# Kernel optimization log

Measured on AMD Instinct MI355X. Metric: run time of the kernel, lower is better.

Reference implementation:

```python
import jax, jax.numpy as jnp
import numpy as np

nC, STEP, ROW = 28, 2, 256
COL = ROW + (nC - 1) * STEP  # 310

# 1/alpha normalization for A_pinv: count of overlapping shifted channels per column
_counts = np.zeros((COL,), np.float32)
for _i in range(nC):
    _counts[_i * STEP:_i * STEP + ROW] += 1.0
ALPHA = jnp.asarray(1.0 / _counts)  # [COL]


def conv1x1(x, w, b):
    # x: [B,C,H,W], w: [O,C], b: [O]
    return jnp.einsum('bchw,oc->bohw', x, w) + b[None, :, None, None]


def dwconv5(x, w, b):
    # depthwise 5x5, SAME padding; w: [C,1,5,5]
    out = jax.lax.conv_general_dilated(
        x, w, window_strides=(1, 1), padding='SAME',
        dimension_numbers=('NCHW', 'OIHW', 'NCHW'),
        feature_group_count=x.shape[1])
    return out + b[None, :, None, None]


def mask_guided(m, w1, b1, w2, b2, dw, db):
    m1 = conv1x1(m, w1, b1)
    attn = jax.nn.sigmoid(dwconv5(conv1x1(m1, w2, b2), dw, db))
    emb = m1 * attn + m1
    return jnp.where(emb == 0, jnp.asarray(1e-6, emb.dtype), emb)


def A_op(x, M):
    # shift-and-add: [B,28,256,256] -> [B,1,256,310]
    z = x * M
    y = jnp.zeros((x.shape[0], 1, ROW, COL), x.dtype)
    for i in range(nC):
        y = y.at[:, :, :, i * STEP:i * STEP + ROW].add(z[:, i:i + 1])
    return y


def A_pinv_op(y, M):
    # normalize then extract shifted windows: [B,1,256,310] -> [B,28,256,256]
    z = y * ALPHA  # broadcast over last dim
    x = jnp.stack([z[:, 0, :, i * STEP:i * STEP + ROW] for i in range(nC)], axis=1)
    return x * M


def setup_inputs() -> dict:
    key = jax.random.key(0)
    ks = jax.random.split(key, 16)
    B = 16
    inp = {
        'y': jax.random.normal(ks[0], (B, 1, ROW, COL), jnp.float32),
        'Phi': jax.random.uniform(ks[1], (B, nC, ROW, ROW), jnp.float32),
        'x_pre': jax.random.normal(ks[2], (B, nC, ROW, ROW), jnp.float32),
        'delta': jnp.asarray([0.1], jnp.float32),
        'mm_w1': jax.random.normal(ks[3], (nC, nC), jnp.float32) * 0.1,
        'mm_b1': jax.random.normal(ks[4], (nC,), jnp.float32) * 0.1,
        'mm_w2': jax.random.normal(ks[5], (nC, nC), jnp.float32) * 0.1,
        'mm_b2': jax.random.normal(ks[6], (nC,), jnp.float32) * 0.1,
        'mm_dw': jax.random.normal(ks[7], (nC, 1, 5, 5), jnp.float32) * 0.1,
        'mm_db': jax.random.normal(ks[8], (nC,), jnp.float32) * 0.1,
        'pv_w1': jax.random.normal(ks[9], (nC, nC), jnp.float32) * 0.1,
        'pv_b1': jax.random.normal(ks[10], (nC,), jnp.float32) * 0.1,
        'pv_w2': jax.random.normal(ks[11], (nC, nC), jnp.float32) * 0.1,
        'pv_b2': jax.random.normal(ks[12], (nC,), jnp.float32) * 0.1,
        'pv_dw': jax.random.normal(ks[13], (nC, 1, 5, 5), jnp.float32) * 0.1,
        'pv_db': jax.random.normal(ks[14], (nC,), jnp.float32) * 0.1,
    }
    return inp


def reference(y, Phi, x_pre, delta,
              mm_w1, mm_b1, mm_w2, mm_b2, mm_dw, mm_db,
              pv_w1, pv_b1, pv_w2, pv_b2, pv_dw, pv_db):
    Phi_learned = mask_guided(Phi, mm_w1, mm_b1, mm_w2, mm_b2, mm_dw, mm_db)
    temp = y - A_op(x_pre, Phi_learned)
    Phi_pinv_learned = mask_guided(Phi, pv_w1, pv_b1, pv_w2, pv_b2, pv_dw, pv_db)
    x_init = x_pre + delta * A_pinv_op(temp, Phi_pinv_learned)
    return x_init
```

## Files before the change

### kernel.cpp

```cpp
#include <hip/hip_runtime.h>
#include <hip/hip_bf16.h>
#include <cstdint>

#define NC 28
#define HW 65536
#define ROWW 256
#define COLW 310
#define BATCH 16

typedef __hip_bfloat16 bf16;

__device__ __forceinline__ float bflo(unsigned int u) { return __uint_as_float(u << 16); }
__device__ __forceinline__ float bfhi(unsigned int u) { return __uint_as_float(u & 0xffff0000u); }
__device__ __forceinline__ unsigned int pk2(float lo, float hi) {
    unsigned short l = __builtin_bit_cast(unsigned short, __float2bfloat16(lo));
    unsigned short h = __builtin_bit_cast(unsigned short, __float2bfloat16(hi));
    return (unsigned int)l | ((unsigned int)h << 16);
}
__device__ __forceinline__ unsigned int pkh(float lo, float hi) {
    auto h = __builtin_amdgcn_cvt_pkrtz(lo, hi);
    return __builtin_bit_cast(unsigned int, h);
}
__device__ __forceinline__ float h2f_lo(unsigned int u) {
    return (float)__builtin_bit_cast(_Float16, (unsigned short)(u & 0xffffu));
}
__device__ __forceinline__ float h2f_hi(unsigned int u) {
    return (float)__builtin_bit_cast(_Float16, (unsigned short)(u >> 16));
}
__device__ __forceinline__ void pkfma16(unsigned int& acc, unsigned int w, unsigned int x) {
    asm("v_pk_fma_f16 %0, %1, %2, %0" : "+v"(acc) : "s"(w), "v"(x));
}

#define REP28A(X) X(0) X(1) X(2) X(3) X(4) X(5) X(6) X(7) X(8) X(9) X(10) X(11) X(12) X(13) \
                  X(14) X(15) X(16) X(17) X(18) X(19) X(20) X(21) X(22) X(23) X(24) X(25) X(26) X(27)

#define HDR_BYTES 16384

__global__ void k0_prep(const float* __restrict__ w1mm, const float* __restrict__ w1pv,
                        const float* __restrict__ w2mm, const float* __restrict__ w2pv,
                        const float* __restrict__ b1mm, const float* __restrict__ b1pv,
                        const float* __restrict__ b2mm, const float* __restrict__ b2pv,
                        const float* __restrict__ dwm,  const float* __restrict__ dwp,
                        const float* __restrict__ dbm,  const float* __restrict__ dbp,
                        unsigned int* __restrict__ hdr)
{
    int t = threadIdx.x;
    for (int e = t; e < 784; e += 256) {
        int c = e / 28, o = e - c * 28;
        hdr[e]       = pkh(w1mm[o * 28 + c], w1pv[o * 28 + c]);
        hdr[784 + e] = pkh(w2mm[e], w2pv[e]);
    }
    if (t < 28) {
        hdr[1568 + t] = pkh(b1mm[t], b1pv[t]);
        hdr[1596 + t] = pkh(b2mm[t], b2pv[t]);
        hdr[2324 + t] = pkh(dbm[t], dbp[t]);
    }
    for (int e = t; e < 700; e += 256)
        hdr[1624 + e] = pkh(dwm[e], dwp[e]);
    float* alpha = (float*)(hdr + 2352);
    for (int col = t; col < COLW; col += 256) {
        int imin = (col > 255) ? ((col - 254) >> 1) : 0;
        int imax = min(27, col >> 1);
        alpha[col] = 1.0f / (float)(imax - imin + 1);
    }
}

__global__ __launch_bounds__(256, 3) void k1_conv1x1(
    const float* __restrict__ Phi, const unsigned int* __restrict__ hdr,
    unsigned int* __restrict__ t_pk, unsigned int* __restrict__ m1_pk)
{
    int idx = blockIdx.x * 256 + threadIdx.x;
    int b   = idx >> 14;
    int hw4 = (idx & 16383) << 2;
    const float* phi = Phi + (size_t)b * NC * HW + hw4;
    const unsigned int* w1h = hdr;
    const unsigned int* w2h = hdr + 784;
    const unsigned int* b1h = hdr + 1568;
    const unsigned int* b2h = hdr + 1596;

#define DECL_M(i) unsigned int MA##i = b1h[i], MB##i = MA##i, MC##i = MA##i, MD##i = MA##i;
    REP28A(DECL_M)
#undef DECL_M

    for (int c = 0; c < NC; c++) {
        float4 P = *reinterpret_cast<const float4*>(phi + (size_t)c * HW);
        unsigned int pa = pkh(P.x, P.x);
        unsigned int pb = pkh(P.y, P.y);
        unsigned int pc = pkh(P.z, P.z);
        unsigned int pd = pkh(P.w, P.w);
        const unsigned int* wr1_ = w1h + c * NC;
#define FMA_M(i) pkfma16(MA##i, wr1_[i], pa); pkfma16(MB##i, wr1_[i], pb); \
                 pkfma16(MC##i, wr1_[i], pc); pkfma16(MD##i, wr1_[i], pd);
        REP28A(FMA_M)
#undef FMA_M
    }

    size_t base = (size_t)b * NC * HW + hw4;
#define ST_M(i) *reinterpret_cast<uint4*>(m1_pk + base + (size_t)(i) * HW) = \
    make_uint4(MA##i, MB##i, MC##i, MD##i);
    REP28A(ST_M)
#undef ST_M

    for (int o = 0; o < NC; o++) {
        const unsigned int* wr2_ = w2h + o * NC;
        unsigned int Ta = b2h[o], Tb = Ta, Tc = Ta, Td = Ta;
#define FMA_T(i) pkfma16(Ta, wr2_[i], MA##i); pkfma16(Tb, wr2_[i], MB##i); \
                 pkfma16(Tc, wr2_[i], MC##i); pkfma16(Td, wr2_[i], MD##i);
        REP28A(FMA_T)
#undef FMA_T
        *reinterpret_cast<uint4*>(t_pk + base + (size_t)o * HW) = make_uint4(Ta, Tb, Tc, Td);
    }
}

#define TR 16
#define LROW 264

#define LDROW(S, LR) do { \
    const uint2* rp_ = reinterpret_cast<const uint2*>(&st[(LR) * LROW + 2 + cc]); \
    uint2 a_ = rp_[0], b_ = rp_[1], c_ = rp_[2]; \
    W##S##0 = a_.x; W##S##1 = a_.y; W##S##2 = b_.x; \
    W##S##3 = b_.y; W##S##4 = c_.x; W##S##5 = c_.y; \
} while(0)

#define PRE(S, R) do { \
    size_t o_ = cbase + (size_t)(h0 + (R)) * 256 + cc; \
    mu##S = *reinterpret_cast<const uint2*>(m1_pk + o_); \
    xp##S = *reinterpret_cast<const float2*>(x_pre + o_); \
} while(0)

#define TAPR(S, B) \
    pkfma16(acc0, wq[(B)+0], W##S##0); pkfma16(acc1, wq[(B)+0], W##S##1); \
    pkfma16(acc0, wq[(B)+1], W##S##1); pkfma16(acc1, wq[(B)+1], W##S##2); \
    pkfma16(acc0, wq[(B)+2], W##S##2); pkfma16(acc1, wq[(B)+2], W##S##3); \
    pkfma16(acc0, wq[(B)+3], W##S##3); pkfma16(acc1, wq[(B)+3], W##S##4); \
    pkfma16(acc0, wq[(B)+4], W##S##4); pkfma16(acc1, wq[(B)+4], W##S##5);

#define CROW2(R, PS, S0,S1,S2,S3,S4) do { \
    unsigned int acc0 = dbc, acc1 = dbc; \
    TAPR(S0, 0) TAPR(S1, 5) TAPR(S2, 10) TAPR(S3, 15) TAPR(S4, 20) \
    float am0 = h2f_lo(acc0), ap0 = h2f_hi(acc0); \
    float am1 = h2f_lo(acc1), ap1 = h2f_hi(acc1); \
    float atm0 = __builtin_amdgcn_rcpf(1.f + __expf(-am0)); \
    float atp0 = __builtin_amdgcn_rcpf(1.f + __expf(-ap0)); \
    float atm1 = __builtin_amdgcn_rcpf(1.f + __expf(-am1)); \
    float atp1 = __builtin_amdgcn_rcpf(1.f + __expf(-ap1)); \
    float m1m0 = h2f_lo(mu##PS.x), m1p0 = h2f_hi(mu##PS.x); \
    float m1m1 = h2f_lo(mu##PS.y), m1p1 = h2f_hi(mu##PS.y); \
    float em0 = fmaf(m1m0, atm0, m1m0); \
    float ep0 = fmaf(m1p0, atp0, m1p0); \
    float em1 = fmaf(m1m1, atm1, m1m1); \
    float ep1 = fmaf(m1p1, atp1, m1p1); \
    if (em0 == 0.f) em0 = 1e-6f; \
    if (ep0 == 0.f) ep0 = 1e-6f; \
    if (em1 == 0.f) em1 = 1e-6f; \
    if (ep1 == 0.f) ep1 = 1e-6f; \
    size_t off_ = cbase + (size_t)(h0 + (R)) * 256 + cc; \
    *reinterpret_cast<unsigned int*>(z + off_)      = pk2(xp##PS.x * em0, xp##PS.y * em1); \
    *reinterpret_cast<unsigned int*>(philpv + off_) = pk2(ep0, ep1); \
} while(0)

__global__ __launch_bounds__(256, 4) void k2_attn(
    const unsigned int* __restrict__ t_pk, const unsigned int* __restrict__ m1_pk,
    const float* __restrict__ x_pre, const unsigned int* __restrict__ hdr,
    bf16* __restrict__ z, bf16* __restrict__ philpv)
{
    __shared__ unsigned int st[(TR + 4) * LROW];

    int bid = blockIdx.x;
    int rt = bid & 15;
    int c  = (bid >> 4) % NC;
    int b  = (bid >> 4) / NC;
    int r0 = rt * TR;
    size_t cbase = ((size_t)b * NC + c) * HW;
    int tid = threadIdx.x;
    int lane = tid & 63;
    int wv = tid >> 6;
    int cc = (tid & 127) * 2;
    int half = tid >> 7;
    int lbase = half * 8;
    int h0 = r0 + lbase;

    if (tid < 80) {
        int rr = tid >> 2, jj = tid & 3;
        st[rr * LROW + ((jj < 2) ? 2 + jj : 258 + jj)] = 0u;
    }

#pragma unroll
    for (int j = 0; j < 5; j++) {
        int r = wv * 5 + j;
        int gr = r0 - 2 + r;
        if (gr >= 0 && gr < 256) {
            const unsigned int* gsrc = t_pk + cbase + (size_t)gr * 256 + lane * 4;
            __builtin_amdgcn_global_load_lds(
                (const __attribute__((address_space(1))) unsigned int*)gsrc,
                (__attribute__((address_space(3))) unsigned int*)&st[r * LROW + 4],
                16, 0, 0);
        } else {
            st[r * LROW + 4 + lane]       = 0u;
            st[r * LROW + 4 + 64 + lane]  = 0u;
            st[r * LROW + 4 + 128 + lane] = 0u;
            st[r * LROW + 4 + 192 + lane] = 0u;
        }
    }

    unsigned int wq[25];
#pragma unroll
    for (int k = 0; k < 25; k++)
        wq[k] = __builtin_amdgcn_readfirstlane(hdr[1624 + c * 25 + k]);
    unsigned int dbc = __builtin_amdgcn_readfirstlane(hdr[2324 + c]);

    uint2  mu0, mu1, mu2, mu3, mu4;
    float2 xp0, xp1, xp2, xp3, xp4;
    PRE(0, 0); PRE(1, 1); PRE(2, 2); PRE(3, 3);

    __syncthreads();

    unsigned int W00,W01,W02,W03,W04,W05, W10,W11,W12,W13,W14,W15,
                 W20,W21,W22,W23,W24,W25, W30,W31,W32,W33,W34,W35,
                 W40,W41,W42,W43,W44,W45;

    LDROW(0, lbase + 0); LDROW(1, lbase + 1); LDROW(2, lbase + 2); LDROW(3, lbase + 3);
    LDROW(4, lbase + 4);  PRE(4, 4);  CROW2(0, 0, 0,1,2,3,4);
    LDROW(0, lbase + 5);  PRE(0, 5);  CROW2(1, 1, 1,2,3,4,0);
    LDROW(1, lbase + 6);  PRE(1, 6);  CROW2(2, 2, 2,3,4,0,1);
    LDROW(2, lbase + 7);  PRE(2, 7);  CROW2(3, 3, 3,4,0,1,2);
    LDROW(3, lbase + 8);              CROW2(4, 4, 4,0,1,2,3);
    LDROW(4, lbase + 9);              CROW2(5, 0, 0,1,2,3,4);
    LDROW(0, lbase + 10);             CROW2(6, 1, 1,2,3,4,0);
    LDROW(1, lbase + 11);             CROW2(7, 2, 2,3,4,0,1);
}

__global__ void k3_aop(const float* __restrict__ y, const bf16* __restrict__ z,
                       const float* __restrict__ alpha, float* __restrict__ temp)
{
    int idx = blockIdx.x * 256 + threadIdx.x;
    if (idx >= BATCH * ROWW * COLW) return;
    int col = idx % COLW;
    int bh  = idx / COLW;
    int h = bh & 255;
    int b = bh >> 8;
    int imin = (col > 255) ? ((col - 254) >> 1) : 0;
    int imax = min(27, col >> 1);
    float acc = y[idx];
    size_t base = (size_t)b * NC * HW + (size_t)h * 256 + col;
    for (int i = imin; i <= imax; i++) {
        acc -= __bfloat162float(z[base + (size_t)i * (HW - 2)]);
    }
    temp[idx] = acc * alpha[col];
}

__global__ void k4_out(const float* __restrict__ x_pre, const bf16* __restrict__ philpv,
                       const float* __restrict__ temp, const float* __restrict__ delta,
                       float* __restrict__ out)
{
    int idx4 = blockIdx.x * 256 + threadIdx.x;
    int wq4 = idx4 & 63;
    int rest = idx4 >> 6;
    int h = rest & 255; rest >>= 8;
    int i = rest % NC;
    int b = rest / NC;
    int w = wq4 * 4;
    int col = w + 2 * i;
    const float* trow = temp + ((size_t)(b * 256 + h)) * COLW + col;
    float t0 = trow[0], t1 = trow[1], t2 = trow[2], t3 = trow[3];
    size_t off = ((size_t)(b * NC + i)) * HW + (size_t)(h * 256 + w);
    uint2 pu = *reinterpret_cast<const uint2*>(philpv + off);
    float4 xp = *reinterpret_cast<const float4*>(x_pre + off);
    float d = delta[0];
    float4 o4;
    o4.x = fmaf(d * t0, bflo(pu.x), xp.x);
    o4.y = fmaf(d * t1, bfhi(pu.x), xp.y);
    o4.z = fmaf(d * t2, bflo(pu.y), xp.z);
    o4.w = fmaf(d * t3, bfhi(pu.y), xp.w);
    *reinterpret_cast<float4*>(out + off) = o4;
}

extern "C" void kernel_launch(void* const* d_in, const int* in_sizes, int n_in,
                              void* d_out, int out_size, void* d_ws, size_t ws_size,
                              hipStream_t stream)
{
    const float* y     = (const float*)d_in[0];
    const float* Phi   = (const float*)d_in[1];
    const float* x_pre = (const float*)d_in[2];
    const float* delta = (const float*)d_in[3];
    const float* mm_w1 = (const float*)d_in[4];
    const float* mm_b1 = (const float*)d_in[5];
    const float* mm_w2 = (const float*)d_in[6];
    const float* mm_b2 = (const float*)d_in[7];
    const float* mm_dw = (const float*)d_in[8];
    const float* mm_db = (const float*)d_in[9];
    const float* pv_w1 = (const float*)d_in[10];
    const float* pv_b1 = (const float*)d_in[11];
    const float* pv_w2 = (const float*)d_in[12];
    const float* pv_b2 = (const float*)d_in[13];
    const float* pv_dw = (const float*)d_in[14];
    const float* pv_db = (const float*)d_in[15];
    float* out = (float*)d_out;

    char* ws = (char*)d_ws;
    const size_t A = (size_t)BATCH * NC * HW * 4;
    unsigned int* hdr    = (unsigned int*)ws;
    unsigned int* t_pk   = (unsigned int*)(ws + HDR_BYTES);
    unsigned int* m1_pk  = (unsigned int*)(ws + HDR_BYTES + A);
    bf16*         zz     = (bf16*)(ws + HDR_BYTES + 2 * A);
    bf16*         philpv = (bf16*)(ws + HDR_BYTES + 2 * A + A / 2);
    float*        temp   = (float*)(ws + HDR_BYTES + 3 * A);
    const float*  alpha  = (const float*)(ws + 2352 * 4);

    k0_prep<<<1, 256, 0, stream>>>(mm_w1, pv_w1, mm_w2, pv_w2,
                                   mm_b1, pv_b1, mm_b2, pv_b2,
                                   mm_dw, pv_dw, mm_db, pv_db, hdr);
    k1_conv1x1<<<1024, 256, 0, stream>>>(Phi, hdr, t_pk, m1_pk);
    k2_attn<<<BATCH * NC * 16, 256, 0, stream>>>(t_pk, m1_pk, x_pre, hdr, zz, philpv);
    k3_aop<<<(BATCH * ROWW * COLW + 255) / 256, 256, 0, stream>>>(y, zz, alpha, temp);
    k4_out<<<(BATCH * NC * HW / 4) / 256, 256, 0, stream>>>(x_pre, philpv, temp, delta, out);
}
```

Measured before the change: 274.0 us.

## Fuse A_op residual and pinv output into one per-row kernel

The separate k3 shift-and-add kernel and k4 output kernel are merged into one kernel, with one block per (batch,row). The block computes the 310-column residual into shared memory and then writes all 28 channel outputs, so the temp buffer no longer makes a global round trip. k2 no longer reads x_pre. It stores the two learned masks as fp16 instead of storing z in bf16, and the fused kernel multiplies x_pre by the mask itself. As a result x_pre is read twice in the fused kernel, the stores are scalar rather than float4, and the precision changes from bf16 to fp16.

```diff
diff --git a/kernel.cpp b/kernel.cpp
--- a/kernel.cpp
+++ b/kernel.cpp
@@ -10,13 +10,6 @@
 
 typedef __hip_bfloat16 bf16;
 
-__device__ __forceinline__ float bflo(unsigned int u) { return __uint_as_float(u << 16); }
-__device__ __forceinline__ float bfhi(unsigned int u) { return __uint_as_float(u & 0xffff0000u); }
-__device__ __forceinline__ unsigned int pk2(float lo, float hi) {
-    unsigned short l = __builtin_bit_cast(unsigned short, __float2bfloat16(lo));
-    unsigned short h = __builtin_bit_cast(unsigned short, __float2bfloat16(hi));
-    return (unsigned int)l | ((unsigned int)h << 16);
-}
 __device__ __forceinline__ unsigned int pkh(float lo, float hi) {
     auto h = __builtin_amdgcn_cvt_pkrtz(lo, hi);
     return __builtin_bit_cast(unsigned int, h);
@@ -26,6 +19,9 @@
 }
 __device__ __forceinline__ float h2f_hi(unsigned int u) {
     return (float)__builtin_bit_cast(_Float16, (unsigned short)(u >> 16));
+}
+__device__ __forceinline__ float h2f(unsigned short u) {
+    return (float)__builtin_bit_cast(_Float16, u);
 }
 __device__ __forceinline__ void pkfma16(unsigned int& acc, unsigned int w, unsigned int x) {
     asm("v_pk_fma_f16 %0, %1, %2, %0" : "+v"(acc) : "s"(w), "v"(x));
@@ -125,7 +121,6 @@
 #define PRE(S, R) do { \
     size_t o_ = cbase + (size_t)(h0 + (R)) * 256 + cc; \
     mu##S = *reinterpret_cast<const uint2*>(m1_pk + o_); \
-    xp##S = *reinterpret_cast<const float2*>(x_pre + o_); \
 } while(0)
 
 #define TAPR(S, B) \
@@ -155,14 +150,14 @@
     if (em1 == 0.f) em1 = 1e-6f; \
     if (ep1 == 0.f) ep1 = 1e-6f; \
     size_t off_ = cbase + (size_t)(h0 + (R)) * 256 + cc; \
-    *reinterpret_cast<unsigned int*>(z + off_)      = pk2(xp##PS.x * em0, xp##PS.y * em1); \
-    *reinterpret_cast<unsigned int*>(philpv + off_) = pk2(ep0, ep1); \
+    *reinterpret_cast<unsigned int*>(phm + off_) = pkh(em0, em1); \
+    *reinterpret_cast<unsigned int*>(php + off_) = pkh(ep0, ep1); \
 } while(0)
 
 __global__ __launch_bounds__(256, 4) void k2_attn(
     const unsigned int* __restrict__ t_pk, const unsigned int* __restrict__ m1_pk,
-    const float* __restrict__ x_pre, const unsigned int* __restrict__ hdr,
-    bf16* __restrict__ z, bf16* __restrict__ philpv)
+    const unsigned int* __restrict__ hdr,
+    unsigned short* __restrict__ phm, unsigned short* __restrict__ php)
 {
     __shared__ unsigned int st[(TR + 4) * LROW];
 
@@ -209,8 +204,7 @@
         wq[k] = __builtin_amdgcn_readfirstlane(hdr[1624 + c * 25 + k]);
     unsigned int dbc = __builtin_amdgcn_readfirstlane(hdr[2324 + c]);
 
-    uint2  mu0, mu1, mu2, mu3, mu4;
-    float2 xp0, xp1, xp2, xp3, xp4;
+    uint2 mu0, mu1, mu2, mu3, mu4;
     PRE(0, 0); PRE(1, 1); PRE(2, 2); PRE(3, 3);
 
     __syncthreads();
@@ -230,49 +224,39 @@
     LDROW(1, lbase + 11);             CROW2(7, 2, 2,3,4,0,1);
 }
 
-__global__ void k3_aop(const float* __restrict__ y, const bf16* __restrict__ z,
-                       const float* __restrict__ alpha, float* __restrict__ temp)
-{
-    int idx = blockIdx.x * 256 + threadIdx.x;
-    if (idx >= BATCH * ROWW * COLW) return;
-    int col = idx % COLW;
-    int bh  = idx / COLW;
-    int h = bh & 255;
-    int b = bh >> 8;
-    int imin = (col > 255) ? ((col - 254) >> 1) : 0;
-    int imax = min(27, col >> 1);
-    float acc = y[idx];
-    size_t base = (size_t)b * NC * HW + (size_t)h * 256 + col;
-    for (int i = imin; i <= imax; i++) {
-        acc -= __bfloat162float(z[base + (size_t)i * (HW - 2)]);
-    }
-    temp[idx] = acc * alpha[col];
-}
-
-__global__ void k4_out(const float* __restrict__ x_pre, const bf16* __restrict__ philpv,
-                       const float* __restrict__ temp, const float* __restrict__ delta,
-                       float* __restrict__ out)
-{
-    int idx4 = blockIdx.x * 256 + threadIdx.x;
-    int wq4 = idx4 & 63;
-    int rest = idx4 >> 6;
-    int h = rest & 255; rest >>= 8;
-    int i = rest % NC;
-    int b = rest / NC;
-    int w = wq4 * 4;
-    int col = w + 2 * i;
-    const float* trow = temp + ((size_t)(b * 256 + h)) * COLW + col;
-    float t0 = trow[0], t1 = trow[1], t2 = trow[2], t3 = trow[3];
-    size_t off = ((size_t)(b * NC + i)) * HW + (size_t)(h * 256 + w);
-    uint2 pu = *reinterpret_cast<const uint2*>(philpv + off);
-    float4 xp = *reinterpret_cast<const float4*>(x_pre + off);
+__global__ __launch_bounds__(256, 8) void k34_out(
+    const float* __restrict__ y, const float* __restrict__ x_pre,
+    const unsigned short* __restrict__ phm, const unsigned short* __restrict__ php,
+    const unsigned int* __restrict__ hdr, const float* __restrict__ delta,
+    float* __restrict__ out)
+{
+    __shared__ float temp[312];
+
+    int tid = threadIdx.x;
+    int b = blockIdx.x >> 8;
+    int h = blockIdx.x & 255;
+    const float* alpha = (const float*)(hdr + 2352);
+    size_t rowbase = ((size_t)b * NC) * HW + (size_t)h * 256;
+    const float* yr = y + ((size_t)b * 256 + h) * COLW;
+
+    for (int col = tid; col < COLW; col += 256) {
+        int imin = (col > 255) ? ((col - 254) >> 1) : 0;
+        int imax = min(27, col >> 1);
+        float acc = yr[col];
+        size_t off = rowbase + (size_t)imin * (HW - 2) + col;
+        for (int i = imin; i <= imax; i++) {
+            acc -= x_pre[off] * h2f(phm[off]);
+            off += (HW - 2);
+        }
+        temp[col] = acc * alpha[col];
+    }
+    __syncthreads();
+
     float d = delta[0];
-    float4 o4;
-    o4.x = fmaf(d * t0, bflo(pu.x), xp.x);
-    o4.y = fmaf(d * t1, bfhi(pu.x), xp.y);
-    o4.z = fmaf(d * t2, bflo(pu.y), xp.z);
-    o4.w = fmaf(d * t3, bfhi(pu.y), xp.w);
-    *reinterpret_cast<float4*>(out + off) = o4;
+    for (int i = 0; i < NC; i++) {
+        size_t off = rowbase + (size_t)i * HW + tid;
+        out[off] = fmaf(d * temp[tid + 2 * i], h2f(php[off]), x_pre[off]);
+    }
 }
 
 extern "C" void kernel_launch(void* const* d_in, const int* in_sizes, int n_in,
@@ -299,19 +283,16 @@
 
     char* ws = (char*)d_ws;
     const size_t A = (size_t)BATCH * NC * HW * 4;
-    unsigned int* hdr    = (unsigned int*)ws;
-    unsigned int* t_pk   = (unsigned int*)(ws + HDR_BYTES);
-    unsigned int* m1_pk  = (unsigned int*)(ws + HDR_BYTES + A);
-    bf16*         zz     = (bf16*)(ws + HDR_BYTES + 2 * A);
-    bf16*         philpv = (bf16*)(ws + HDR_BYTES + 2 * A + A / 2);
-    float*        temp   = (float*)(ws + HDR_BYTES + 3 * A);
-    const float*  alpha  = (const float*)(ws + 2352 * 4);
+    unsigned int*   hdr   = (unsigned int*)ws;
+    unsigned int*   t_pk  = (unsigned int*)(ws + HDR_BYTES);
+    unsigned int*   m1_pk = (unsigned int*)(ws + HDR_BYTES + A);
+    unsigned short* phm   = (unsigned short*)(ws + HDR_BYTES + 2 * A);
+    unsigned short* php   = (unsigned short*)(ws + HDR_BYTES + 2 * A + A / 2);
 
     k0_prep<<<1, 256, 0, stream>>>(mm_w1, pv_w1, mm_w2, pv_w2,
                                    mm_b1, pv_b1, mm_b2, pv_b2,
                                    mm_dw, pv_dw, mm_db, pv_db, hdr);
     k1_conv1x1<<<1024, 256, 0, stream>>>(Phi, hdr, t_pk, m1_pk);
-    k2_attn<<<BATCH * NC * 16, 256, 0, stream>>>(t_pk, m1_pk, x_pre, hdr, zz, philpv);
-    k3_aop<<<(BATCH * ROWW * COLW + 255) / 256, 256, 0, stream>>>(y, zz, alpha, temp);
-    k4_out<<<(BATCH * NC * HW / 4) / 256, 256, 0, stream>>>(x_pre, philpv, temp, delta, out);
-}
+    k2_attn<<<BATCH * NC * 16, 256, 0, stream>>>(t_pk, m1_pk, hdr, phm, php);
+    k34_out<<<BATCH * 256, 256, 0, stream>>>(y, x_pre, phm, php, hdr, delta, out);
+}
```

Result: faster. 258.2 us (-5.8%).
